# Kernel tuning notes

Measured on AMD Instinct MI355X. Metric: run time of the kernel, lower is better.

The kernel has to match this reference:

```python
import jax, jax.numpy as jnp
import numpy as np

B, N, D, U = 8, 2048, 512, 128


def setup_inputs() -> dict:
    key = jax.random.key(0)
    k_x, k_q, k_k, k_v, k_o = jax.random.split(key, 5)
    scale_in = 1.0 / np.sqrt(D)
    scale_u = 1.0 / np.sqrt(U)
    return {
        "inputs": jax.random.normal(k_x, (B, N, D), dtype=jnp.float32),
        "W_q": jax.random.normal(k_q, (D, U), dtype=jnp.float32) * scale_in,
        "W_k": jax.random.normal(k_k, (D, U), dtype=jnp.float32) * scale_in,
        "W_v": jax.random.normal(k_v, (D, U), dtype=jnp.float32) * scale_in,
        "W_o": jax.random.normal(k_o, (U, D), dtype=jnp.float32) * scale_u,
        "b_o": jnp.zeros((D,), dtype=jnp.float32),
    }


def reference(inputs, W_q, W_k, W_v, W_o, b_o):
    # Single-head scaled dot-product self-attention + output dense + residual
    Q = jnp.einsum('bnd,du->bnu', inputs, W_q)
    K = jnp.einsum('bnd,du->bnu', inputs, W_k)
    V = jnp.einsum('bnd,du->bnu', inputs, W_v)
    inv_sqrt_u = 1.0 / jnp.sqrt(jnp.asarray(W_q.shape[-1], inputs.dtype))
    scores = jnp.einsum('bnu,bmu->bnm', Q, K) * inv_sqrt_u  # [B,N,N]
    attn = jax.nn.softmax(scores, axis=-1)
    ctx = jnp.einsum('bnm,bmu->bnu', attn, V)  # [B,N,U]
    return jnp.einsum('bnu,ud->bnd', ctx, W_o) + b_o + inputs
```

## Files before the change

### kernel.cpp

```cpp
#include <hip/hip_runtime.h>

#define BB 8
#define NN 2048
#define DD 512
#define UU 128
#define SPLITS 8
#define KSPLIT 256

typedef __bf16 bf16_t;
typedef __bf16 bf16x4 __attribute__((ext_vector_type(4)));
typedef __bf16 bf16x8 __attribute__((ext_vector_type(8)));
typedef float floatx4 __attribute__((ext_vector_type(4)));

__device__ __forceinline__ floatx4 mfma16(bf16x8 a, bf16x8 b, floatx4 c) {
  return __builtin_amdgcn_mfma_f32_16x16x32_bf16(a, b, c, 0, 0, 0);
}

#define SW(r, g) ((((g) ^ ((r) & 7)) * 8))

__device__ __forceinline__ void gld_lds16(const bf16_t* g, bf16_t* l) {
  __builtin_amdgcn_global_load_lds(
      (const __attribute__((address_space(1))) unsigned int*)g,
      (__attribute__((address_space(3))) unsigned int*)l, 16, 0, 0);
}

__global__ __launch_bounds__(256) void cast_x_kernel(const float* __restrict__ x,
                                                     bf16_t* __restrict__ xb) {
  int G = blockIdx.x * 256 + threadIdx.x;
  int token = G >> 6;
  int g = G & 63;
  int dstg = (g & 56) | ((g & 7) ^ (token & 7));
  const float4* src = reinterpret_cast<const float4*>(x) + (size_t)G * 2;
  float4 a = src[0], b = src[1];
  bf16x8 o;
  o[0] = (bf16_t)a.x; o[1] = (bf16_t)a.y; o[2] = (bf16_t)a.z; o[3] = (bf16_t)a.w;
  o[4] = (bf16_t)b.x; o[5] = (bf16_t)b.y; o[6] = (bf16_t)b.z; o[7] = (bf16_t)b.w;
  *reinterpret_cast<bf16x8*>(&xb[(size_t)token * 512 + dstg * 8]) = o;
}

__global__ __launch_bounds__(256) void pack_w_kernel(const float* __restrict__ wq,
                                                     const float* __restrict__ wk,
                                                     const float* __restrict__ wv,
                                                     const float* __restrict__ wo,
                                                     bf16_t* __restrict__ wqkvt,
                                                     bf16_t* __restrict__ wot) {
  int gid = blockIdx.x * 256 + threadIdx.x;
  if (gid < 384 * 512) {
    int nrow = gid >> 9;
    int kdst = gid & 511;
    int ksrc = (kdst & ~56) | (((((kdst >> 3) & 7)) ^ (nrow & 7)) << 3);
    const float* src = (nrow < 128) ? wq : ((nrow < 256) ? wk : wv);
    int n = nrow & 127;
    wqkvt[gid] = (bf16_t)src[ksrc * 128 + n];
  } else {
    int g = gid - 384 * 512;
    int nrow = g >> 7;
    int kdst = g & 127;
    int ksrc = (kdst & ~56) | (((((kdst >> 3) & 7)) ^ (nrow & 7)) << 3);
    wot[g] = (bf16_t)wo[ksrc * 512 + nrow];
  }
}

__global__ __launch_bounds__(256, 4) void qkv_gemm_kernel(const bf16_t* __restrict__ xb,
                                                          const bf16_t* __restrict__ wqkvt,
                                                          bf16_t* __restrict__ Q,
                                                          bf16_t* __restrict__ K,
                                                          bf16_t* __restrict__ Vt) {
  __shared__ bf16_t lA[64 * 64];
  __shared__ bf16_t lB[64 * 64];
  const int m0 = blockIdx.x * 64;
  const int n0 = blockIdx.y * 64;
  const int tid = threadIdx.x;
  const int w = tid >> 6, lane = tid & 63;
  const int quad = lane >> 4, l15 = lane & 15;

  floatx4 zero4 = {0.f, 0.f, 0.f, 0.f};
  floatx4 acc[4];
#pragma unroll
  for (int nt = 0; nt < 4; nt++) acc[nt] = zero4;

  for (int kc = 0; kc < 512; kc += 64) {
    __syncthreads();
#pragma unroll
    for (int i = 0; i < 2; i++) {
      int t = tid + i * 256;
      int r = t >> 3, g = t & 7;
      gld_lds16(&xb[(size_t)(m0 + r) * 512 + kc + g * 8], &lA[t * 8]);
      gld_lds16(&wqkvt[(size_t)(n0 + r) * 512 + kc + g * 8], &lB[t * 8]);
    }
    asm volatile("s_waitcnt vmcnt(0)" ::: "memory");
    __syncthreads();
#pragma unroll
    for (int kb = 0; kb < 2; kb++) {
      bf16x8 a = *reinterpret_cast<const bf16x8*>(&lA[(w * 16 + l15) * 64 + SW(l15, kb * 4 + quad)]);
#pragma unroll
      for (int nt = 0; nt < 4; nt++) {
        bf16x8 b = *reinterpret_cast<const bf16x8*>(&lB[(nt * 16 + l15) * 64 + SW(l15, kb * 4 + quad)]);
        acc[nt] = mfma16(a, b, acc[nt]);
      }
    }
  }

#pragma unroll
  for (int nt = 0; nt < 4; nt++) {
    int n = n0 + nt * 16 + l15;
#pragma unroll
    for (int r = 0; r < 4; r++) {
      int token = m0 + w * 16 + quad * 4 + r;
      bf16_t h = (bf16_t)acc[nt][r];
      if (n < 128) {
        Q[(size_t)token * 128 + n] = h;
      } else if (n < 256) {
        int nk = n - 128;
        int nsw = (nk & ~56) | ((((nk >> 3) & 7) ^ (token & 7)) << 3);
        K[(size_t)token * 128 + nsw] = h;
      } else {
        int b = token >> 11;
        int t = token & 2047;
        int u = n - 256;
        int tsw = (t & ~56) | ((((t >> 3) & 7) ^ (u & 7)) << 3);
        Vt[((size_t)b * 128 + u) * 2048 + tsw] = h;
      }
    }
  }
}

__global__ __launch_bounds__(256, 3) void attn_kernel(const bf16_t* __restrict__ Q,
                                                      const bf16_t* __restrict__ K,
                                                      const bf16_t* __restrict__ Vt,
                                                      bf16_t* __restrict__ Op,
                                                      float* __restrict__ ml) {
  __shared__ bf16_t lK[64 * 128];
  __shared__ bf16_t lV[128 * 64];
  __shared__ bf16_t lP[4][32 * 64];

  const int b = blockIdx.y;
  const int qb = blockIdx.x;
  const int s = blockIdx.z;
  const int tid = threadIdx.x;
  const int w = tid >> 6, lane = tid & 63;
  const int quad = lane >> 4, l15 = lane & 15;
  const float c = 0.08838834764831845f * 1.4426950408889634f;

  bf16x8 qf[2][4];
#pragma unroll
  for (int mt = 0; mt < 2; mt++) {
    const bf16_t* qrow =
        &Q[((size_t)b * NN + qb * 128 + w * 32 + mt * 16 + l15) * 128 + quad * 8];
#pragma unroll
    for (int kb = 0; kb < 4; kb++)
      qf[mt][kb] = *reinterpret_cast<const bf16x8*>(qrow + kb * 32);
  }

  float l_part[2] = {0.f, 0.f};
  floatx4 zero4 = {0.f, 0.f, 0.f, 0.f};
  floatx4 accO[2][8];
#pragma unroll
  for (int mt = 0; mt < 2; mt++)
#pragma unroll
    for (int ut = 0; ut < 8; ut++) accO[mt][ut] = zero4;

  bf16_t* pw = &lP[w][0];
  const int kt0 = s * KSPLIT;
  for (int kt = kt0; kt < kt0 + KSPLIT; kt += 64) {
    __syncthreads();
    {
      const bf16_t* ksrc = &K[((size_t)b * NN + kt) * 128];
#pragma unroll
      for (int i = 0; i < 4; i++) {
        int t = tid + i * 256;
        gld_lds16(ksrc + (size_t)t * 8, &lK[t * 8]);
      }
      const bf16_t* vbase = &Vt[(size_t)b * 128 * 2048 + kt];
#pragma unroll
      for (int i = 0; i < 4; i++) {
        int t = tid + i * 256;
        int r = t >> 3, g = t & 7;
        gld_lds16(vbase + (size_t)r * 2048 + g * 8, &lV[t * 8]);
      }
    }
    asm volatile("s_waitcnt vmcnt(0)" ::: "memory");
    __syncthreads();

    floatx4 accS[4][2];
#pragma unroll
    for (int km = 0; km < 4; km++)
#pragma unroll
      for (int mt = 0; mt < 2; mt++) accS[km][mt] = zero4;
#pragma unroll
    for (int kb = 0; kb < 4; kb++) {
#pragma unroll
      for (int km = 0; km < 4; km++) {
        bf16x8 kf = *reinterpret_cast<const bf16x8*>(
            &lK[(km * 16 + l15) * 128 + SW(l15, kb * 4 + quad)]);
#pragma unroll
        for (int mt = 0; mt < 2; mt++)
          accS[km][mt] = mfma16(kf, qf[mt][kb], accS[km][mt]);
      }
    }

#pragma unroll
    for (int km = 0; km < 4; km++) {
#pragma unroll
      for (int mt = 0; mt < 2; mt++) {
        float p0 = __builtin_amdgcn_exp2f(accS[km][mt][0] * c);
        float p1 = __builtin_amdgcn_exp2f(accS[km][mt][1] * c);
        float p2 = __builtin_amdgcn_exp2f(accS[km][mt][2] * c);
        float p3 = __builtin_amdgcn_exp2f(accS[km][mt][3] * c);
        l_part[mt] += (p0 + p1) + (p2 + p3);
        bf16x4 pk;
        pk[0] = (bf16_t)p0; pk[1] = (bf16_t)p1; pk[2] = (bf16_t)p2; pk[3] = (bf16_t)p3;
        int row = mt * 16 + l15;
        int g = km * 2 + (quad >> 1);
        *reinterpret_cast<bf16x4*>(
            &pw[row * 64 + ((g ^ (row & 7)) * 8) + (quad & 1) * 4]) = pk;
      }
    }
    asm volatile("s_waitcnt lgkmcnt(0)" ::: "memory");

#pragma unroll
    for (int kb = 0; kb < 2; kb++) {
      bf16x8 pa[2];
#pragma unroll
      for (int mt = 0; mt < 2; mt++)
        pa[mt] = *reinterpret_cast<const bf16x8*>(
            &pw[(mt * 16 + l15) * 64 + SW(l15, kb * 4 + quad)]);
#pragma unroll
      for (int ut = 0; ut < 8; ut++) {
        bf16x8 bv = *reinterpret_cast<const bf16x8*>(
            &lV[(ut * 16 + l15) * 64 + SW(l15, kb * 4 + quad)]);
#pragma unroll
        for (int mt = 0; mt < 2; mt++)
          accO[mt][ut] = mfma16(pa[mt], bv, accO[mt][ut]);
      }
    }
  }

#pragma unroll
  for (int mt = 0; mt < 2; mt++) {
    float v = l_part[mt];
    v += __shfl_xor(v, 16);
    v += __shfl_xor(v, 32);
    l_part[mt] = v;
  }

  size_t base = ((size_t)(b * 16 + qb) * SPLITS + s);
  bf16_t* op = Op + base * (128 * 128);
  float* mlp = ml + base * 128;
#pragma unroll
  for (int mt = 0; mt < 2; mt++)
#pragma unroll
    for (int ut = 0; ut < 8; ut++)
#pragma unroll
      for (int r = 0; r < 4; r++)
        op[(w * 32 + mt * 16 + quad * 4 + r) * 128 + ut * 16 + l15] =
            (bf16_t)accO[mt][ut][r];
  if (quad == 0) {
#pragma unroll
    for (int mt = 0; mt < 2; mt++) mlp[w * 32 + mt * 16 + l15] = l_part[mt];
  }
}

__global__ __launch_bounds__(256) void merge_kernel(const bf16_t* __restrict__ Op,
                                                    const float* __restrict__ ml,
                                                    bf16_t* __restrict__ ctx) {
  const int blk = blockIdx.x;
  const int q = threadIdx.x >> 1;
  const int u0 = blockIdx.y * 64 + (threadIdx.x & 1) * 32;

  float L = 0.f;
  float o[32];
#pragma unroll
  for (int j = 0; j < 32; j++) o[j] = 0.f;
#pragma unroll
  for (int s = 0; s < SPLITS; s++) {
    L += ml[((size_t)blk * SPLITS + s) * 128 + q];
    const bf16_t* op = Op + ((size_t)blk * SPLITS + s) * 16384 + q * 128 + u0;
#pragma unroll
    for (int v = 0; v < 4; v++) {
      bf16x8 ch = *reinterpret_cast<const bf16x8*>(op + v * 8);
#pragma unroll
      for (int j = 0; j < 8; j++) o[v * 8 + j] += (float)ch[j];
    }
  }
  float inv = 1.0f / L;
  const int bb = blk >> 4, qbl = blk & 15;
  bf16_t* dst = ctx + ((size_t)bb * NN + qbl * 128 + q) * 128;
#pragma unroll
  for (int v = 0; v < 4; v++) {
    int g = (u0 >> 3) + v;
    int gsw = (g & 8) | ((g & 7) ^ (q & 7));
    bf16x8 ch;
#pragma unroll
    for (int j = 0; j < 8; j++) ch[j] = (bf16_t)(o[v * 8 + j] * inv);
    *reinterpret_cast<bf16x8*>(dst + gsw * 8) = ch;
  }
}

__global__ __launch_bounds__(256, 4) void out_gemm_kernel(const bf16_t* __restrict__ ctx,
                                                          const bf16_t* __restrict__ wot,
                                                          const float* __restrict__ bo,
                                                          const float* __restrict__ x0,
                                                          float* __restrict__ out) {
  __shared__ bf16_t lA[64 * 128];
  __shared__ bf16_t lB[64 * 128];
  const int m0 = blockIdx.x * 64;
  const int n0 = blockIdx.y * 64;
  const int tid = threadIdx.x;
  const int w = tid >> 6, lane = tid & 63;
  const int quad = lane >> 4, l15 = lane & 15;

#pragma unroll
  for (int i = 0; i < 4; i++) {
    int t = tid + i * 256;
    gld_lds16(&ctx[(size_t)m0 * 128 + t * 8], &lA[t * 8]);
    gld_lds16(&wot[(size_t)n0 * 128 + t * 8], &lB[t * 8]);
  }
  asm volatile("s_waitcnt vmcnt(0)" ::: "memory");
  __syncthreads();

  floatx4 zero4 = {0.f, 0.f, 0.f, 0.f};
  floatx4 acc[4];
#pragma unroll
  for (int nt = 0; nt < 4; nt++) acc[nt] = zero4;
#pragma unroll
  for (int kb = 0; kb < 4; kb++) {
    bf16x8 a = *reinterpret_cast<const bf16x8*>(&lA[(w * 16 + l15) * 128 + SW(l15, kb * 4 + quad)]);
#pragma unroll
    for (int nt = 0; nt < 4; nt++) {
      bf16x8 bfr = *reinterpret_cast<const bf16x8*>(&lB[(nt * 16 + l15) * 128 + SW(l15, kb * 4 + quad)]);
      acc[nt] = mfma16(a, bfr, acc[nt]);
    }
  }

#pragma unroll
  for (int nt = 0; nt < 4; nt++) {
    int n = n0 + nt * 16 + l15;
    float bias = bo[n];
#pragma unroll
    for (int r = 0; r < 4; r++) {
      size_t m = m0 + w * 16 + quad * 4 + r;
      out[m * 512 + n] = acc[nt][r] + bias + x0[m * 512 + n];
    }
  }
}

extern "C" void kernel_launch(void* const* d_in, const int* in_sizes, int n_in,
                              void* d_out, int out_size, void* d_ws, size_t ws_size,
                              hipStream_t stream) {
  const float* x  = (const float*)d_in[0];
  const float* wq = (const float*)d_in[1];
  const float* wk = (const float*)d_in[2];
  const float* wv = (const float*)d_in[3];
  const float* wo = (const float*)d_in[4];
  const float* bo = (const float*)d_in[5];
  float* out = (float*)d_out;

  char* ws = (char*)d_ws;
  bf16_t* Qb    = (bf16_t*)(ws);
  bf16_t* Kb    = (bf16_t*)(ws + 4194304);
  bf16_t* Vt    = (bf16_t*)(ws + 2 * 4194304);
  bf16_t* Ctx   = (bf16_t*)(ws + 3 * 4194304);
  bf16_t* Wqkvt = (bf16_t*)(ws + 4 * 4194304);
  bf16_t* Wot   = (bf16_t*)(ws + 4 * 4194304 + 393216);
  bf16_t* Xb    = (bf16_t*)(ws + 4 * 4194304 + 524288);
  bf16_t* Op    = (bf16_t*)(ws + 4 * 4194304 + 524288);
  float*  ml    = (float*)(ws + 4 * 4194304 + 524288 + 33554432);

  cast_x_kernel<<<4096, 256, 0, stream>>>(x, Xb);
  pack_w_kernel<<<1024, 256, 0, stream>>>(wq, wk, wv, wo, Wqkvt, Wot);
  qkv_gemm_kernel<<<dim3(256, 6), 256, 0, stream>>>(Xb, Wqkvt, Qb, Kb, Vt);
  attn_kernel<<<dim3(16, 8, SPLITS), 256, 0, stream>>>(Qb, Kb, Vt, Op, ml);
  merge_kernel<<<dim3(128, 2), 256, 0, stream>>>(Op, ml, Ctx);
  out_gemm_kernel<<<dim3(256, 8), 256, 0, stream>>>(Ctx, Wot, bo, x, out);
}
```

Measured before the change: 162.4 us.

## Double-buffer attention K/V tiles and enlarge QKV GEMM tiles to 128x128

The attention kernel now uses 32-key tiles held in two LDS buffers and prefetches the next K/V tile with async global-to-LDS loads while computing on the current one. A partial vmcnt wait and raw barriers replace the full drain. The Vt swizzle and P layout change to fit the narrower tile. Separately, the QKV projection GEMM moves from 64x64 to 128x128 block tiles with a 4x4 MFMA accumulator per wave, for more operand reuse at the cost of fewer blocks and lower occupancy.

```diff
diff --git a/kernel.cpp b/kernel.cpp
--- a/kernel.cpp
+++ b/kernel.cpp
@@ -6,6 +6,7 @@
 #define UU 128
 #define SPLITS 8
 #define KSPLIT 256
+#define TK 32
 
 typedef __bf16 bf16_t;
 typedef __bf16 bf16x4 __attribute__((ext_vector_type(4)));
@@ -61,65 +62,84 @@
   }
 }
 
-__global__ __launch_bounds__(256, 4) void qkv_gemm_kernel(const bf16_t* __restrict__ xb,
+__global__ __launch_bounds__(256, 2) void qkv_gemm_kernel(const bf16_t* __restrict__ xb,
                                                           const bf16_t* __restrict__ wqkvt,
                                                           bf16_t* __restrict__ Q,
                                                           bf16_t* __restrict__ K,
                                                           bf16_t* __restrict__ Vt) {
-  __shared__ bf16_t lA[64 * 64];
-  __shared__ bf16_t lB[64 * 64];
-  const int m0 = blockIdx.x * 64;
-  const int n0 = blockIdx.y * 64;
+  __shared__ bf16_t lA[128 * 64];
+  __shared__ bf16_t lB[128 * 64];
+  const int m0 = blockIdx.x * 128;
+  const int n0 = blockIdx.y * 128;
   const int tid = threadIdx.x;
   const int w = tid >> 6, lane = tid & 63;
   const int quad = lane >> 4, l15 = lane & 15;
+  const int mh = (w & 1) * 64, nh = (w >> 1) * 64;
 
   floatx4 zero4 = {0.f, 0.f, 0.f, 0.f};
-  floatx4 acc[4];
-#pragma unroll
-  for (int nt = 0; nt < 4; nt++) acc[nt] = zero4;
+  floatx4 acc[4][4];
+#pragma unroll
+  for (int mt = 0; mt < 4; mt++)
+#pragma unroll
+    for (int nt = 0; nt < 4; nt++) acc[mt][nt] = zero4;
 
   for (int kc = 0; kc < 512; kc += 64) {
     __syncthreads();
 #pragma unroll
-    for (int i = 0; i < 2; i++) {
-      int t = tid + i * 256;
-      int r = t >> 3, g = t & 7;
-      gld_lds16(&xb[(size_t)(m0 + r) * 512 + kc + g * 8], &lA[t * 8]);
-      gld_lds16(&wqkvt[(size_t)(n0 + r) * 512 + kc + g * 8], &lB[t * 8]);
+    for (int i = 0; i < 4; i++) {
+      int G = tid + i * 256;
+      int r = G >> 3, g = G & 7;
+      gld_lds16(&xb[(size_t)(m0 + r) * 512 + kc + g * 8], &lA[G * 8]);
+    }
+#pragma unroll
+    for (int i = 0; i < 4; i++) {
+      int G = tid + i * 256;
+      int r = G >> 3, g = G & 7;
+      gld_lds16(&wqkvt[(size_t)(n0 + r) * 512 + kc + g * 8], &lB[G * 8]);
     }
     asm volatile("s_waitcnt vmcnt(0)" ::: "memory");
     __syncthreads();
 #pragma unroll
     for (int kb = 0; kb < 2; kb++) {
-      bf16x8 a = *reinterpret_cast<const bf16x8*>(&lA[(w * 16 + l15) * 64 + SW(l15, kb * 4 + quad)]);
-#pragma unroll
-      for (int nt = 0; nt < 4; nt++) {
-        bf16x8 b = *reinterpret_cast<const bf16x8*>(&lB[(nt * 16 + l15) * 64 + SW(l15, kb * 4 + quad)]);
-        acc[nt] = mfma16(a, b, acc[nt]);
-      }
+      bf16x8 af[4], bfr[4];
+#pragma unroll
+      for (int mt = 0; mt < 4; mt++)
+        af[mt] = *reinterpret_cast<const bf16x8*>(
+            &lA[(mh + mt * 16 + l15) * 64 + SW(l15, kb * 4 + quad)]);
+#pragma unroll
+      for (int nt = 0; nt < 4; nt++)
+        bfr[nt] = *reinterpret_cast<const bf16x8*>(
+            &lB[(nh + nt * 16 + l15) * 64 + SW(l15, kb * 4 + quad)]);
+#pragma unroll
+      for (int mt = 0; mt < 4; mt++)
+#pragma unroll
+        for (int nt = 0; nt < 4; nt++)
+          acc[mt][nt] = mfma16(af[mt], bfr[nt], acc[mt][nt]);
     }
   }
 
 #pragma unroll
   for (int nt = 0; nt < 4; nt++) {
-    int n = n0 + nt * 16 + l15;
-#pragma unroll
-    for (int r = 0; r < 4; r++) {
-      int token = m0 + w * 16 + quad * 4 + r;
-      bf16_t h = (bf16_t)acc[nt][r];
-      if (n < 128) {
-        Q[(size_t)token * 128 + n] = h;
-      } else if (n < 256) {
-        int nk = n - 128;
-        int nsw = (nk & ~56) | ((((nk >> 3) & 7) ^ (token & 7)) << 3);
-        K[(size_t)token * 128 + nsw] = h;
-      } else {
-        int b = token >> 11;
-        int t = token & 2047;
-        int u = n - 256;
-        int tsw = (t & ~56) | ((((t >> 3) & 7) ^ (u & 7)) << 3);
-        Vt[((size_t)b * 128 + u) * 2048 + tsw] = h;
+    int n = n0 + nh + nt * 16 + l15;
+#pragma unroll
+    for (int mt = 0; mt < 4; mt++) {
+#pragma unroll
+      for (int r = 0; r < 4; r++) {
+        int token = m0 + mh + mt * 16 + quad * 4 + r;
+        bf16_t h = (bf16_t)acc[mt][nt][r];
+        if (n < 128) {
+          Q[(size_t)token * 128 + n] = h;
+        } else if (n < 256) {
+          int nk = n - 128;
+          int nsw = (nk & ~56) | ((((nk >> 3) & 7) ^ (token & 7)) << 3);
+          K[(size_t)token * 128 + nsw] = h;
+        } else {
+          int bb = token >> 11;
+          int t = token & 2047;
+          int u = n - 256;
+          int tsw = (t & ~24) | ((((t >> 3) & 3) ^ (u & 3)) << 3);
+          Vt[((size_t)bb * 128 + u) * 2048 + tsw] = h;
+        }
       }
     }
   }
@@ -130,9 +150,9 @@
                                                       const bf16_t* __restrict__ Vt,
                                                       bf16_t* __restrict__ Op,
                                                       float* __restrict__ ml) {
-  __shared__ bf16_t lK[64 * 128];
-  __shared__ bf16_t lV[128 * 64];
-  __shared__ bf16_t lP[4][32 * 64];
+  __shared__ bf16_t lK[2][TK * 128];
+  __shared__ bf16_t lV[2][128 * TK];
+  __shared__ bf16_t lP[4][32 * TK];
 
   const int b = blockIdx.y;
   const int qb = blockIdx.x;
@@ -162,37 +182,57 @@
 
   bf16_t* pw = &lP[w][0];
   const int kt0 = s * KSPLIT;
-  for (int kt = kt0; kt < kt0 + KSPLIT; kt += 64) {
-    __syncthreads();
-    {
-      const bf16_t* ksrc = &K[((size_t)b * NN + kt) * 128];
-#pragma unroll
-      for (int i = 0; i < 4; i++) {
-        int t = tid + i * 256;
-        gld_lds16(ksrc + (size_t)t * 8, &lK[t * 8]);
+  const bf16_t* kbase = &K[((size_t)b * NN + kt0) * 128];
+  const bf16_t* vbase = &Vt[(size_t)b * 128 * 2048 + kt0];
+
+  {
+#pragma unroll
+    for (int i = 0; i < 2; i++) {
+      int G = tid + i * 256;
+      gld_lds16(kbase + (size_t)G * 8, &lK[0][G * 8]);
+    }
+#pragma unroll
+    for (int i = 0; i < 2; i++) {
+      int G = tid + i * 256;
+      gld_lds16(vbase + (size_t)(G >> 2) * 2048 + (G & 3) * 8, &lV[0][G * 8]);
+    }
+  }
+
+  for (int it = 0; it < KSPLIT / TK; it++) {
+    const int buf = it & 1;
+    if (it < KSPLIT / TK - 1) {
+      const int nb = buf ^ 1;
+      const bf16_t* ks = kbase + (size_t)(it + 1) * TK * 128;
+      const bf16_t* vs = vbase + (it + 1) * TK;
+#pragma unroll
+      for (int i = 0; i < 2; i++) {
+        int G = tid + i * 256;
+        gld_lds16(ks + (size_t)G * 8, &lK[nb][G * 8]);
       }
-      const bf16_t* vbase = &Vt[(size_t)b * 128 * 2048 + kt];
-#pragma unroll
-      for (int i = 0; i < 4; i++) {
-        int t = tid + i * 256;
-        int r = t >> 3, g = t & 7;
-        gld_lds16(vbase + (size_t)r * 2048 + g * 8, &lV[t * 8]);
+#pragma unroll
+      for (int i = 0; i < 2; i++) {
+        int G = tid + i * 256;
+        gld_lds16(vs + (size_t)(G >> 2) * 2048 + (G & 3) * 8, &lV[nb][G * 8]);
       }
-    }
-    asm volatile("s_waitcnt vmcnt(0)" ::: "memory");
-    __syncthreads();
-
-    floatx4 accS[4][2];
-#pragma unroll
-    for (int km = 0; km < 4; km++)
+      asm volatile("s_waitcnt vmcnt(4)" ::: "memory");
+    } else {
+      asm volatile("s_waitcnt vmcnt(0)" ::: "memory");
+    }
+    asm volatile("s_barrier" ::: "memory");
+
+    floatx4 accS[2][2];
+#pragma unroll
+    for (int km = 0; km < 2; km++)
 #pragma unroll
       for (int mt = 0; mt < 2; mt++) accS[km][mt] = zero4;
 #pragma unroll
     for (int kb = 0; kb < 4; kb++) {
 #pragma unroll
-      for (int km = 0; km < 4; km++) {
+      for (int km = 0; km < 2; km++) {
+        int g = kb * 4 + quad;
+        int gs = (g & 8) | ((g & 7) ^ (l15 & 7));
         bf16x8 kf = *reinterpret_cast<const bf16x8*>(
-            &lK[(km * 16 + l15) * 128 + SW(l15, kb * 4 + quad)]);
+            &lK[buf][(km * 16 + l15) * 128 + gs * 8]);
 #pragma unroll
         for (int mt = 0; mt < 2; mt++)
           accS[km][mt] = mfma16(kf, qf[mt][kb], accS[km][mt]);
@@ -200,7 +240,7 @@
     }
 
 #pragma unroll
-    for (int km = 0; km < 4; km++) {
+    for (int km = 0; km < 2; km++) {
 #pragma unroll
       for (int mt = 0; mt < 2; mt++) {
         float p0 = __builtin_amdgcn_exp2f(accS[km][mt][0] * c);
@@ -210,30 +250,27 @@
         l_part[mt] += (p0 + p1) + (p2 + p3);
         bf16x4 pk;
         pk[0] = (bf16_t)p0; pk[1] = (bf16_t)p1; pk[2] = (bf16_t)p2; pk[3] = (bf16_t)p3;
-        int row = mt * 16 + l15;
-        int g = km * 2 + (quad >> 1);
-        *reinterpret_cast<bf16x4*>(
-            &pw[row * 64 + ((g ^ (row & 7)) * 8) + (quad & 1) * 4]) = pk;
+        int q = mt * 16 + l15;
+        int gk = (km * 2 + (quad >> 1)) ^ (q & 3);
+        *reinterpret_cast<bf16x4*>(&pw[q * TK + gk * 8 + (quad & 1) * 4]) = pk;
       }
     }
     asm volatile("s_waitcnt lgkmcnt(0)" ::: "memory");
 
-#pragma unroll
-    for (int kb = 0; kb < 2; kb++) {
-      bf16x8 pa[2];
+    bf16x8 pa[2];
+#pragma unroll
+    for (int mt = 0; mt < 2; mt++)
+      pa[mt] = *reinterpret_cast<const bf16x8*>(
+          &pw[(mt * 16 + l15) * TK + (quad ^ (l15 & 3)) * 8]);
+#pragma unroll
+    for (int ut = 0; ut < 8; ut++) {
+      bf16x8 bv = *reinterpret_cast<const bf16x8*>(
+          &lV[buf][(ut * 16 + l15) * TK + (quad ^ (l15 & 3)) * 8]);
 #pragma unroll
       for (int mt = 0; mt < 2; mt++)
-        pa[mt] = *reinterpret_cast<const bf16x8*>(
-            &pw[(mt * 16 + l15) * 64 + SW(l15, kb * 4 + quad)]);
-#pragma unroll
-      for (int ut = 0; ut < 8; ut++) {
-        bf16x8 bv = *reinterpret_cast<const bf16x8*>(
-            &lV[(ut * 16 + l15) * 64 + SW(l15, kb * 4 + quad)]);
-#pragma unroll
-        for (int mt = 0; mt < 2; mt++)
-          accO[mt][ut] = mfma16(pa[mt], bv, accO[mt][ut]);
-      }
-    }
+        accO[mt][ut] = mfma16(pa[mt], bv, accO[mt][ut]);
+    }
+    asm volatile("s_barrier" ::: "memory");
   }
 
 #pragma unroll
@@ -369,7 +406,7 @@
 
   cast_x_kernel<<<4096, 256, 0, stream>>>(x, Xb);
   pack_w_kernel<<<1024, 256, 0, stream>>>(wq, wk, wv, wo, Wqkvt, Wot);
-  qkv_gemm_kernel<<<dim3(256, 6), 256, 0, stream>>>(Xb, Wqkvt, Qb, Kb, Vt);
+  qkv_gemm_kernel<<<dim3(128, 3), 256, 0, stream>>>(Xb, Wqkvt, Qb, Kb, Vt);
   attn_kernel<<<dim3(16, 8, SPLITS), 256, 0, stream>>>(Qb, Kb, Vt, Op, ml);
   merge_kernel<<<dim3(128, 2), 256, 0, stream>>>(Op, ml, Ctx);
   out_gemm_kernel<<<dim3(256, 8), 256, 0, stream>>>(Ctx, Wot, bo, x, out);
```

Result: no change. 164.5 us (+1.3%).
